# Kernel optimization log

Hardware: AMD Instinct MI355X
Metric: run time of the kernel (lower is better)

The kernel has to match this reference:

```python
import jax, jax.numpy as jnp
import numpy as np

B, C1, C2, H, W = 16, 64, 64, 160, 160
K, KS, HID = 4, 3, 16  # K kernels, 3x3, hidden = max(int(64/16),16)=16
EPS = 1e-5


def setup_inputs() -> dict:
    key = jax.random.key(0)
    ks = jax.random.split(key, 8)
    fan_out = KS * KS * C2
    return {
        "x": jax.random.normal(ks[0], (B, C1, H, W), jnp.float32),
        # K candidate conv kernels and biases
        "Wk": jax.random.normal(ks[1], (K, C2, C1, KS, KS), jnp.float32) * np.sqrt(2.0 / fan_out),
        "bk": jnp.zeros((K, C2), jnp.float32),
        # attention trunk: 1x1 conv C1->HID (no bias), BN, ReLU
        "Wfc": jax.random.normal(ks[2], (HID, C1), jnp.float32) * 0.1,
        "gamma_h": jnp.ones((HID,), jnp.float32),
        "beta_h": jnp.zeros((HID,), jnp.float32),
        # four attention heads
        "Wf": jax.random.normal(ks[3], (C2, HID), jnp.float32) * 0.1,
        "bf": jnp.zeros((C2,), jnp.float32),
        "Ws": jax.random.normal(ks[4], (KS * KS, HID), jnp.float32) * 0.1,
        "bs": jnp.zeros((KS * KS,), jnp.float32),
        "Wc": jax.random.normal(ks[5], (C1, HID), jnp.float32) * 0.1,
        "bc": jnp.zeros((C1,), jnp.float32),
        "Ww": jax.random.normal(ks[6], (K, HID), jnp.float32) * 0.1,
        "bw": jnp.zeros((K,), jnp.float32),
        # outer BatchNorm2d params
        "gamma_o": jnp.ones((C2,), jnp.float32),
        "beta_o": jnp.zeros((C2,), jnp.float32),
    }


def reference(x, Wk, bk, Wfc, gamma_h, beta_h, Wf, bf, Ws, bs, Wc, bc, Ww, bw, gamma_o, beta_o):
    # ---- per-sample attention over K kernels ----
    ctx = x.mean(axis=(2, 3))                      # (B, C1)  global avg pool
    h = ctx @ Wfc.T                                # (B, HID) 1x1 conv == linear
    mu = h.mean(axis=0)
    var = h.var(axis=0)                            # biased, as torch BN training
    h = (h - mu) / jnp.sqrt(var + EPS) * gamma_h + beta_h
    h = jax.nn.relu(h)
    attn_f = jax.nn.sigmoid(h @ Wf.T + bf)         # (B, C2)
    attn_s = jax.nn.sigmoid(h @ Ws.T + bs).reshape(B, KS, KS)
    attn_c = jax.nn.sigmoid(h @ Wc.T + bc)         # (B, C1)
    attn_w = jax.nn.softmax(h @ Ww.T + bw, axis=-1)  # (B, K)

    # attn: (B, K, C2, C1, KS, KS) via broadcasting
    attn = (attn_w[:, :, None, None, None, None]
            * attn_f[:, None, :, None, None, None]
            * attn_c[:, None, None, :, None, None]
            * attn_s[:, None, None, None, :, :])
    weight = jnp.sum(attn * Wk[None], axis=1)      # (B, C2, C1, KS, KS)
    bias = attn_w @ bk                             # (B, C2)

    # ---- batched conv as grouped conv with groups=B ----
    out = jax.lax.conv_general_dilated(
        x.reshape(1, B * C1, H, W),
        weight.reshape(B * C2, C1, KS, KS),
        window_strides=(1, 1), padding=((1, 1), (1, 1)),
        dimension_numbers=('NCHW', 'OIHW', 'NCHW'),
        feature_group_count=B)                     # (1, B*C2, H, W)
    out = out.reshape(B, C2, H, W) + bias[:, :, None, None]

    # ---- outer BatchNorm2d (training stats) + SiLU ----
    mu_o = out.mean(axis=(0, 2, 3))
    var_o = out.var(axis=(0, 2, 3))
    out = (out - mu_o[None, :, None, None]) / jnp.sqrt(var_o + EPS)[None, :, None, None]
    out = out * gamma_o[None, :, None, None] + beta_o[None, :, None, None]
    return out * jax.nn.sigmoid(out)               # SiLU
```

## Files before the change

kernel.cpp:

```cpp
#include <hip/hip_runtime.h>
#include <math.h>

#define BB 16
#define C1 64
#define C2 64
#define HH 160
#define WW 160
#define KK 4
#define HID 16
#define EPS 1e-5f
#define HWSZ (HH*WW)
#define NPB (BB*HWSZ)

#define WS_AF    1024
#define WS_AC    2048
#define WS_AS    3072
#define WS_AW    3216
#define WS_BIAS  3280
#define WS_SC    4304
#define WS_SH    4368
#define WS_STATS 4432
#define NSLOT    32
#define WS_PART  8704
#define WS_WEFF  49664
#define WS_XBF   344576

typedef __attribute__((ext_vector_type(8)))  short bf16x8;
typedef __attribute__((ext_vector_type(16))) float f32x16;

__device__ __forceinline__ unsigned short f2bf(float f) {
    unsigned int u = __float_as_uint(f);
    unsigned int r = (u + 0x7FFFu + ((u >> 16) & 1u)) >> 16;
    return (unsigned short)r;
}

__device__ __forceinline__ void gload16(const void* g, void* l) {
    __builtin_amdgcn_global_load_lds(
        (const __attribute__((address_space(1))) unsigned int*)g,
        (__attribute__((address_space(3))) unsigned int*)l, 16, 0, 0);
}

__global__ __launch_bounds__(256) void xprep_kernel(const float* __restrict__ x,
                                                    float* __restrict__ ws) {
    __shared__ float lds[10240];
    int bcc = blockIdx.y;
    int rg = blockIdx.x;
    int t = threadIdx.x;

    const float* src = x + (size_t)bcc * 16 * HWSZ + (size_t)rg * 4 * WW;
    float4* l4 = (float4*)lds;
    #pragma unroll
    for (int i = 0; i < 10; ++i) {
        int g = i * 256 + t;
        int ch = g / 160, rem = g - ch * 160;
        l4[g] = *(const float4*)(src + (size_t)ch * HWSZ + rem * 4);
    }
    __syncthreads();

    {
        int ch = t >> 4, j = t & 15;
        float s = 0.f;
        #pragma unroll
        for (int m = 0; m < 40; ++m) s += lds[ch * 640 + j + 16 * m];
        #pragma unroll
        for (int o = 8; o > 0; o >>= 1) s += __shfl_down(s, o, 16);
        if (j == 0) ws[WS_PART + ((size_t)bcc * 40 + rg) * 16 + ch] = s;
    }

    uint4* dst = (uint4*)(ws + WS_XBF) + ((size_t)bcc * 160 + rg * 4) * 320;
    #pragma unroll
    for (int i = 0; i < 5; ++i) {
        int u = i * 256 + t;
        int row = u / 320, rem = u - row * 320;
        int col = rem >> 1, p = rem & 1;
        int h = p ^ ((col >> 2) & 1) ^ 1;
        union { uint4 q; unsigned short us[8]; } pk;
        #pragma unroll
        for (int k = 0; k < 8; ++k)
            pk.us[k] = f2bf(lds[(h * 8 + k) * 640 + row * 160 + col]);
        dst[u] = pk.q;
    }
}

__global__ void attn_kernel(float* __restrict__ ws,
    const float* __restrict__ Wfc, const float* __restrict__ gh, const float* __restrict__ bh,
    const float* __restrict__ Wf,  const float* __restrict__ bf,
    const float* __restrict__ Wsm, const float* __restrict__ bs,
    const float* __restrict__ Wc,  const float* __restrict__ bc,
    const float* __restrict__ Ww,  const float* __restrict__ bw,
    const float* __restrict__ bk) {
    __shared__ float ctxs[16][64];
    __shared__ float hs[16][16];
    __shared__ float aw[16][4];
    int t = threadIdx.x;

    #pragma unroll
    for (int q = 0; q < 4; ++q) {
        int idx = t * 4 + q;
        int b = idx >> 6, c1 = idx & 63;
        const float* pp = ws + WS_PART + ((size_t)(b * 4 + (c1 >> 4)) * 40) * 16 + (c1 & 15);
        float s = 0.f;
        #pragma unroll
        for (int rg = 0; rg < 40; ++rg) s += pp[rg * 16];
        ctxs[b][c1] = s * (1.0f / (float)HWSZ);
    }
    __syncthreads();
    {
        int b = t >> 4, j = t & 15;
        const float* wr = Wfc + j * 64;
        float s = 0.f;
        #pragma unroll
        for (int c = 0; c < 64; c++) s += ctxs[b][c] * wr[c];
        hs[b][j] = s;
    }
    __syncthreads();
    if (t < 16) {
        int j = t;
        float mu = 0.f;
        #pragma unroll
        for (int b = 0; b < 16; b++) mu += hs[b][j];
        mu *= (1.f / 16.f);
        float vr = 0.f;
        #pragma unroll
        for (int b = 0; b < 16; b++) { float d = hs[b][j] - mu; vr += d * d; }
        vr *= (1.f / 16.f);
        float sc = gh[j] * rsqrtf(vr + EPS);
        float sh = bh[j] - mu * sc;
        #pragma unroll
        for (int b = 0; b < 16; b++) {
            float v = hs[b][j] * sc + sh;
            hs[b][j] = v > 0.f ? v : 0.f;
        }
    }
    __syncthreads();
    if (t < 16) {
        int b = t;
        float l[4]; float mx = -1e30f;
        #pragma unroll
        for (int k = 0; k < 4; k++) {
            float s = bw[k];
            #pragma unroll
            for (int j = 0; j < 16; j++) s += hs[b][j] * Ww[k * 16 + j];
            l[k] = s; mx = fmaxf(mx, s);
        }
        float den = 0.f;
        #pragma unroll
        for (int k = 0; k < 4; k++) { l[k] = expf(l[k] - mx); den += l[k]; }
        float r = 1.f / den;
        #pragma unroll
        for (int k = 0; k < 4; k++) { float v = l[k] * r; aw[b][k] = v; ws[WS_AW + b * 4 + k] = v; }
    }
    #pragma unroll
    for (int q = 0; q < 4; q++) {
        int idx = t * 4 + q;
        int b = idx >> 6, c2 = idx & 63;
        float sf = bf[c2], sc2 = bc[c2];
        #pragma unroll
        for (int j = 0; j < 16; j++) {
            float hv = hs[b][j];
            sf  += hv * Wf[c2 * 16 + j];
            sc2 += hv * Wc[c2 * 16 + j];
        }
        ws[WS_AF + idx] = 1.f / (1.f + expf(-sf));
        ws[WS_AC + idx] = 1.f / (1.f + expf(-sc2));
    }
    if (t < 144) {
        int b = t / 9, uv = t % 9;
        float s = bs[uv];
        #pragma unroll
        for (int j = 0; j < 16; j++) s += hs[b][j] * Wsm[uv * 16 + j];
        ws[WS_AS + t] = 1.f / (1.f + expf(-s));
    }
    __syncthreads();
    #pragma unroll
    for (int q = 0; q < 4; q++) {
        int idx = t * 4 + q;
        int b = idx >> 6, c2 = idx & 63;
        float s = 0.f;
        #pragma unroll
        for (int k = 0; k < 4; k++) s += aw[b][k] * bk[k * 64 + c2];
        ws[WS_BIAS + idx] = s;
    }
    for (int i = t; i < NSLOT * 128; i += 256) ws[WS_STATS + i] = 0.f;
}

__global__ void wprep_kernel(const float* __restrict__ Wk, float* __restrict__ ws) {
    int b = blockIdx.y;
    int tid = blockIdx.x * 256 + threadIdx.x;
    int h = tid & 1;
    int c2 = (tid >> 1) & 63;
    int g = tid >> 7;
    int uv = g % 9;
    int chunk = g / 9;
    const float* awp = ws + WS_AW + b * 4;
    float aw0 = awp[0], aw1 = awp[1], aw2 = awp[2], aw3 = awp[3];
    float af = ws[WS_AF + b * 64 + c2];
    float as_ = ws[WS_AS + b * 9 + uv];
    union { uint4 q; unsigned short u[8]; } pk;
    #pragma unroll
    for (int j = 0; j < 8; ++j) {
        int c1 = chunk * 16 + h * 8 + j;
        const float* wp = Wk + (size_t)(c2 * 64 + c1) * 9 + uv;
        float s = aw0 * wp[0] + aw1 * wp[64 * 64 * 9] + aw2 * wp[2 * 64 * 64 * 9] + aw3 * wp[3 * 64 * 64 * 9];
        float w = s * af * ws[WS_AC + b * 64 + c1] * as_;
        pk.u[j] = f2bf(w);
    }
    int unit = ((chunk * 9 + uv) * 64 + c2) * 2 + (h ^ ((c2 >> 2) & 1));
    ((uint4*)(ws + WS_WEFF))[(size_t)b * 4608 + unit] = pk.q;
}

__launch_bounds__(256, 2)
__global__ void conv_kernel(const float* __restrict__ wsf, float* __restrict__ out) {
    __shared__ uint4 xs[6 * 162 * 2];
    __shared__ uint4 wsh[2][1152];
    __shared__ float bsh[64];
    __shared__ float sst[128];

    int id = blockIdx.x;
    int b = id & 15;
    int bx = id >> 4;
    int y0 = bx * 4;
    int t = threadIdx.x;
    int wv = t >> 6;
    int lane = t & 63;
    int l31 = lane & 31;
    int l5 = lane >> 5;

    if (t < 64) bsh[t] = wsf[WS_BIAS + b * 64 + t];
    if (t >= 64 && t < 128) sst[t - 64] = 0.f;
    if (t >= 128 && t < 192) sst[t - 64] = 0.f;
    if (t >= 192 && t < 216) {
        int q = t - 192;
        int r = q >> 2, side = (q >> 1) & 1, p = q & 1;
        xs[(r * 162 + side * 161) * 2 + p] = make_uint4(0, 0, 0, 0);
    }
    int rbad = (bx == 0) ? 0 : (bx == 39 ? 5 : -1);
    if (rbad >= 0) {
        for (int i = t; i < 320; i += 256)
            xs[(rbad * 162 + 1) * 2 + i] = make_uint4(0, 0, 0, 0);
    }

    const uint4* weff = (const uint4*)(wsf + WS_WEFF) + (size_t)b * 4608;
    const uint4* xbf  = (const uint4*)(wsf + WS_XBF);

    auto stage_w = [&](int cc, int bq) {
        for (int i = wv; i < 18; i += 4)
            gload16(weff + (size_t)cc * 1152 + i * 64 + lane, (char*)&wsh[bq][0] + i * 1024);
    };
    auto stage_x = [&](int cc) {
        for (int i = wv; i < 30; i += 4) {
            int r = i / 5, seg = i % 5;
            int gy = y0 - 1 + r;
            if (gy >= 0 && gy < HH)
                gload16(xbf + (((size_t)b * 4 + cc) * 160 + gy) * 320 + seg * 64 + lane,
                        (char*)xs + ((r * 162 + 1) * 2 + seg * 64) * 16);
        }
    };

    f32x16 acc[2][5];
    #pragma unroll
    for (int a = 0; a < 2; ++a)
        #pragma unroll
        for (int j = 0; j < 5; ++j)
            #pragma unroll
            for (int r = 0; r < 16; ++r) acc[a][j][r] = 0.f;

    stage_w(0, 0);
    stage_x(0);
    __syncthreads();

    int cur = 0;
    int aswz = (l31 >> 2) & 1;
    for (int cc = 0; cc < 4; ++cc) {
        if (cc < 3) stage_w(cc + 1, cur ^ 1);
        #pragma unroll
        for (int uv = 0; uv < 9; ++uv) {
            bf16x8 a0 = *(bf16x8*)&wsh[cur][(uv * 64 + l31) * 2 + (l5 ^ aswz)];
            bf16x8 a1 = *(bf16x8*)&wsh[cur][(uv * 64 + 32 + l31) * 2 + (l5 ^ aswz)];
            int xrow = wv + uv / 3;
            int v = uv % 3;
            #pragma unroll
            for (int j = 0; j < 5; ++j) {
                int col = j * 32 + l31 + v;
                bf16x8 bb = *(bf16x8*)&xs[(xrow * 162 + col) * 2 + (l5 ^ (((col + 3) >> 2) & 1))];
                acc[0][j] = __builtin_amdgcn_mfma_f32_32x32x16_bf16(a0, bb, acc[0][j], 0, 0, 0);
                acc[1][j] = __builtin_amdgcn_mfma_f32_32x32x16_bf16(a1, bb, acc[1][j], 0, 0, 0);
            }
        }
        __syncthreads();
        if (cc < 3) stage_x(cc + 1);
        __syncthreads();
        cur ^= 1;
    }

    float* outb = out + (size_t)b * C2 * HWSZ + (size_t)(y0 + wv) * WW;
    #pragma unroll
    for (int a = 0; a < 2; ++a) {
        float sr[16], qr[16];
        #pragma unroll
        for (int r = 0; r < 16; ++r) {
            int c2r = a * 32 + (r & 3) + 8 * (r >> 2) + 4 * l5;
            float bias = bsh[c2r];
            float s = 0.f, q = 0.f;
            #pragma unroll
            for (int j = 0; j < 5; ++j) {
                float v = acc[a][j][r] + bias;
                outb[(size_t)c2r * HWSZ + j * 32 + l31] = v;
                s += v;
                q = fmaf(v, v, q);
            }
            sr[r] = s; qr[r] = q;
        }
        #pragma unroll
        for (int k = 0; k < 4; ++k) {
            int m = 1 << k, n = 8 >> k;
            #pragma unroll
            for (int i = 0; i < 8; ++i) {
                if (i < n) {
                    float ks = (l31 & m) ? sr[i + n] : sr[i];
                    float ss = (l31 & m) ? sr[i] : sr[i + n];
                    sr[i] = ks + __shfl_xor(ss, m, 64);
                    float kq = (l31 & m) ? qr[i + n] : qr[i];
                    float sq = (l31 & m) ? qr[i] : qr[i + n];
                    qr[i] = kq + __shfl_xor(sq, m, 64);
                }
            }
        }
        sr[0] += __shfl_xor(sr[0], 16, 64);
        qr[0] += __shfl_xor(qr[0], 16, 64);
        if (l31 < 16) {
            int rf = ((l31 & 1) << 3) | ((l31 & 2) << 1) | ((l31 & 4) >> 1) | ((l31 & 8) >> 3);
            int c2r = a * 32 + (rf & 3) + 8 * (rf >> 2) + 4 * l5;
            atomicAdd(&sst[c2r], sr[0]);
            atomicAdd(&sst[64 + c2r], qr[0]);
        }
    }
    __syncthreads();
    if (t < 128) {
        int slot = id & (NSLOT - 1);
        atomicAdd((float*)wsf + WS_STATS + slot * 128 + t, sst[t]);
    }
}

__global__ void bnstat_kernel(float* __restrict__ ws, const float* __restrict__ go,
                              const float* __restrict__ bo) {
    int c = threadIdx.x;
    float s = 0.f, q = 0.f;
    for (int sl = 0; sl < NSLOT; sl++) {
        s += ws[WS_STATS + sl * 128 + c];
        q += ws[WS_STATS + sl * 128 + 64 + c];
    }
    float mu  = s * (1.0f / (float)NPB);
    float var = q * (1.0f / (float)NPB) - mu * mu;
    float sc  = go[c] * rsqrtf(var + EPS);
    ws[WS_SC + c] = sc;
    ws[WS_SH + c] = bo[c] - mu * sc;
}

__global__ void bnact_kernel(float* __restrict__ out, const float* __restrict__ ws) {
    __shared__ float sc[64], sh[64];
    if (threadIdx.x < 64) {
        sc[threadIdx.x] = ws[WS_SC + threadIdx.x];
        sh[threadIdx.x] = ws[WS_SH + threadIdx.x];
    }
    __syncthreads();
    const int n4 = BB * C2 * HWSZ / 4;
    for (int i = blockIdx.x * blockDim.x + threadIdx.x; i < n4; i += gridDim.x * blockDim.x) {
        float4 v = ((float4*)out)[i];
        int c = ((i * 4) / HWSZ) & 63;
        float s = sc[c], h = sh[c];
        v.x = v.x * s + h; v.y = v.y * s + h; v.z = v.z * s + h; v.w = v.w * s + h;
        v.x = v.x / (1.f + __expf(-v.x));
        v.y = v.y / (1.f + __expf(-v.y));
        v.z = v.z / (1.f + __expf(-v.z));
        v.w = v.w / (1.f + __expf(-v.w));
        ((float4*)out)[i] = v;
    }
}

extern "C" void kernel_launch(void* const* d_in, const int* in_sizes, int n_in,
                              void* d_out, int out_size, void* d_ws, size_t ws_size,
                              hipStream_t stream) {
    const float* x   = (const float*)d_in[0];
    const float* Wk  = (const float*)d_in[1];
    const float* bk  = (const float*)d_in[2];
    const float* Wfc = (const float*)d_in[3];
    const float* gh  = (const float*)d_in[4];
    const float* bh  = (const float*)d_in[5];
    const float* Wf  = (const float*)d_in[6];
    const float* bf  = (const float*)d_in[7];
    const float* Wsm = (const float*)d_in[8];
    const float* bs  = (const float*)d_in[9];
    const float* Wc  = (const float*)d_in[10];
    const float* bc  = (const float*)d_in[11];
    const float* Ww  = (const float*)d_in[12];
    const float* bw  = (const float*)d_in[13];
    const float* go  = (const float*)d_in[14];
    const float* bo  = (const float*)d_in[15];
    float* out = (float*)d_out;
    float* ws  = (float*)d_ws;

    xprep_kernel<<<dim3(40, 64), dim3(256), 0, stream>>>(x, ws);
    attn_kernel<<<dim3(1), dim3(256), 0, stream>>>(ws, Wfc, gh, bh, Wf, bf, Wsm, bs, Wc, bc, Ww, bw, bk);
    wprep_kernel<<<dim3(18, 16), dim3(256), 0, stream>>>(Wk, ws);
    conv_kernel<<<dim3(640), dim3(256), 0, stream>>>(ws, out);
    bnstat_kernel<<<dim3(1), dim3(64), 0, stream>>>(ws, go, bo);
    bnact_kernel<<<dim3(2048), dim3(256), 0, stream>>>(out, ws);
}
```

Baseline: 132.4 us.

## Halve conv tile rows, split output channels across waves, drop double buffering

Measured after the change: 131.4 us. No clear change (-0.7%).

```diff
diff --git a/kernel.cpp b/kernel.cpp
--- a/kernel.cpp
+++ b/kernel.cpp
@@ -209,32 +209,33 @@
     ((uint4*)(ws + WS_WEFF))[(size_t)b * 4608 + unit] = pk.q;
 }
 
-__launch_bounds__(256, 2)
+__launch_bounds__(256, 3)
 __global__ void conv_kernel(const float* __restrict__ wsf, float* __restrict__ out) {
-    __shared__ uint4 xs[6 * 162 * 2];
-    __shared__ uint4 wsh[2][1152];
+    __shared__ uint4 xs[4 * 162 * 2];
+    __shared__ uint4 wsh[1152];
     __shared__ float bsh[64];
     __shared__ float sst[128];
 
     int id = blockIdx.x;
     int b = id & 15;
     int bx = id >> 4;
-    int y0 = bx * 4;
+    int y0 = bx * 2;
     int t = threadIdx.x;
     int wv = t >> 6;
     int lane = t & 63;
     int l31 = lane & 31;
     int l5 = lane >> 5;
+    int c2h = wv & 1;
+    int rw = wv >> 1;
 
     if (t < 64) bsh[t] = wsf[WS_BIAS + b * 64 + t];
-    if (t >= 64 && t < 128) sst[t - 64] = 0.f;
-    if (t >= 128 && t < 192) sst[t - 64] = 0.f;
-    if (t >= 192 && t < 216) {
+    if (t >= 64 && t < 192) sst[t - 64] = 0.f;
+    if (t >= 192 && t < 208) {
         int q = t - 192;
         int r = q >> 2, side = (q >> 1) & 1, p = q & 1;
         xs[(r * 162 + side * 161) * 2 + p] = make_uint4(0, 0, 0, 0);
     }
-    int rbad = (bx == 0) ? 0 : (bx == 39 ? 5 : -1);
+    int rbad = (bx == 0) ? 0 : (bx == 79 ? 3 : -1);
     if (rbad >= 0) {
         for (int i = t; i < 320; i += 256)
             xs[(rbad * 162 + 1) * 2 + i] = make_uint4(0, 0, 0, 0);
@@ -243,97 +244,80 @@
     const uint4* weff = (const uint4*)(wsf + WS_WEFF) + (size_t)b * 4608;
     const uint4* xbf  = (const uint4*)(wsf + WS_XBF);
 
-    auto stage_w = [&](int cc, int bq) {
+    f32x16 acc[5];
+    #pragma unroll
+    for (int j = 0; j < 5; ++j)
+        #pragma unroll
+        for (int r = 0; r < 16; ++r) acc[j][r] = 0.f;
+
+    int c2 = c2h * 32 + l31;
+    int aswz = (l31 >> 2) & 1;
+    for (int cc = 0; cc < 4; ++cc) {
+        __syncthreads();
         for (int i = wv; i < 18; i += 4)
-            gload16(weff + (size_t)cc * 1152 + i * 64 + lane, (char*)&wsh[bq][0] + i * 1024);
-    };
-    auto stage_x = [&](int cc) {
-        for (int i = wv; i < 30; i += 4) {
+            gload16(weff + (size_t)cc * 1152 + i * 64 + lane, (char*)wsh + i * 1024);
+        for (int i = wv; i < 20; i += 4) {
             int r = i / 5, seg = i % 5;
             int gy = y0 - 1 + r;
             if (gy >= 0 && gy < HH)
                 gload16(xbf + (((size_t)b * 4 + cc) * 160 + gy) * 320 + seg * 64 + lane,
                         (char*)xs + ((r * 162 + 1) * 2 + seg * 64) * 16);
         }
-    };
-
-    f32x16 acc[2][5];
-    #pragma unroll
-    for (int a = 0; a < 2; ++a)
-        #pragma unroll
-        for (int j = 0; j < 5; ++j)
-            #pragma unroll
-            for (int r = 0; r < 16; ++r) acc[a][j][r] = 0.f;
-
-    stage_w(0, 0);
-    stage_x(0);
-    __syncthreads();
-
-    int cur = 0;
-    int aswz = (l31 >> 2) & 1;
-    for (int cc = 0; cc < 4; ++cc) {
-        if (cc < 3) stage_w(cc + 1, cur ^ 1);
+        __syncthreads();
+
         #pragma unroll
         for (int uv = 0; uv < 9; ++uv) {
-            bf16x8 a0 = *(bf16x8*)&wsh[cur][(uv * 64 + l31) * 2 + (l5 ^ aswz)];
-            bf16x8 a1 = *(bf16x8*)&wsh[cur][(uv * 64 + 32 + l31) * 2 + (l5 ^ aswz)];
-            int xrow = wv + uv / 3;
+            bf16x8 a = *(bf16x8*)&wsh[(uv * 64 + c2) * 2 + (l5 ^ aswz)];
+            int xr = rw + uv / 3;
             int v = uv % 3;
             #pragma unroll
             for (int j = 0; j < 5; ++j) {
                 int col = j * 32 + l31 + v;
-                bf16x8 bb = *(bf16x8*)&xs[(xrow * 162 + col) * 2 + (l5 ^ (((col + 3) >> 2) & 1))];
-                acc[0][j] = __builtin_amdgcn_mfma_f32_32x32x16_bf16(a0, bb, acc[0][j], 0, 0, 0);
-                acc[1][j] = __builtin_amdgcn_mfma_f32_32x32x16_bf16(a1, bb, acc[1][j], 0, 0, 0);
+                bf16x8 bb = *(bf16x8*)&xs[(xr * 162 + col) * 2 + (l5 ^ (((col + 3) >> 2) & 1))];
+                acc[j] = __builtin_amdgcn_mfma_f32_32x32x16_bf16(a, bb, acc[j], 0, 0, 0);
             }
         }
-        __syncthreads();
-        if (cc < 3) stage_x(cc + 1);
-        __syncthreads();
-        cur ^= 1;
-    }
-
-    float* outb = out + (size_t)b * C2 * HWSZ + (size_t)(y0 + wv) * WW;
-    #pragma unroll
-    for (int a = 0; a < 2; ++a) {
-        float sr[16], qr[16];
-        #pragma unroll
-        for (int r = 0; r < 16; ++r) {
-            int c2r = a * 32 + (r & 3) + 8 * (r >> 2) + 4 * l5;
-            float bias = bsh[c2r];
-            float s = 0.f, q = 0.f;
-            #pragma unroll
-            for (int j = 0; j < 5; ++j) {
-                float v = acc[a][j][r] + bias;
-                outb[(size_t)c2r * HWSZ + j * 32 + l31] = v;
-                s += v;
-                q = fmaf(v, v, q);
+    }
+
+    float* outb = out + (size_t)b * C2 * HWSZ + (size_t)(y0 + rw) * WW;
+    int cb = c2h * 32 + 4 * l5;
+    float sr[16], qr[16];
+    #pragma unroll
+    for (int r = 0; r < 16; ++r) {
+        int c2r = cb + (r & 3) + 8 * (r >> 2);
+        float bias = bsh[c2r];
+        float s = 0.f, q = 0.f;
+        #pragma unroll
+        for (int j = 0; j < 5; ++j) {
+            float v = acc[j][r] + bias;
+            outb[(size_t)c2r * HWSZ + j * 32 + l31] = v;
+            s += v;
+            q = fmaf(v, v, q);
+        }
+        sr[r] = s; qr[r] = q;
+    }
+    #pragma unroll
+    for (int k = 0; k < 4; ++k) {
+        int m = 1 << k, n = 8 >> k;
+        #pragma unroll
+        for (int i = 0; i < 8; ++i) {
+            if (i < n) {
+                float ks = (l31 & m) ? sr[i + n] : sr[i];
+                float ss = (l31 & m) ? sr[i] : sr[i + n];
+                sr[i] = ks + __shfl_xor(ss, m, 64);
+                float kq = (l31 & m) ? qr[i + n] : qr[i];
+                float sq = (l31 & m) ? qr[i] : qr[i + n];
+                qr[i] = kq + __shfl_xor(sq, m, 64);
             }
-            sr[r] = s; qr[r] = q;
-        }
-        #pragma unroll
-        for (int k = 0; k < 4; ++k) {
-            int m = 1 << k, n = 8 >> k;
-            #pragma unroll
-            for (int i = 0; i < 8; ++i) {
-                if (i < n) {
-                    float ks = (l31 & m) ? sr[i + n] : sr[i];
-                    float ss = (l31 & m) ? sr[i] : sr[i + n];
-                    sr[i] = ks + __shfl_xor(ss, m, 64);
-                    float kq = (l31 & m) ? qr[i + n] : qr[i];
-                    float sq = (l31 & m) ? qr[i] : qr[i + n];
-                    qr[i] = kq + __shfl_xor(sq, m, 64);
-                }
-            }
-        }
-        sr[0] += __shfl_xor(sr[0], 16, 64);
-        qr[0] += __shfl_xor(qr[0], 16, 64);
-        if (l31 < 16) {
-            int rf = ((l31 & 1) << 3) | ((l31 & 2) << 1) | ((l31 & 4) >> 1) | ((l31 & 8) >> 3);
-            int c2r = a * 32 + (rf & 3) + 8 * (rf >> 2) + 4 * l5;
-            atomicAdd(&sst[c2r], sr[0]);
-            atomicAdd(&sst[64 + c2r], qr[0]);
-        }
+        }
+    }
+    sr[0] += __shfl_xor(sr[0], 16, 64);
+    qr[0] += __shfl_xor(qr[0], 16, 64);
+    if (l31 < 16) {
+        int rf = ((l31 & 1) << 3) | ((l31 & 2) << 1) | ((l31 & 4) >> 1) | ((l31 & 8) >> 3);
+        int c2r = cb + (rf & 3) + 8 * (rf >> 2);
+        atomicAdd(&sst[c2r], sr[0]);
+        atomicAdd(&sst[64 + c2r], qr[0]);
     }
     __syncthreads();
     if (t < 128) {
@@ -403,7 +387,7 @@
     xprep_kernel<<<dim3(40, 64), dim3(256), 0, stream>>>(x, ws);
     attn_kernel<<<dim3(1), dim3(256), 0, stream>>>(ws, Wfc, gh, bh, Wf, bf, Wsm, bs, Wc, bc, Ww, bw, bk);
     wprep_kernel<<<dim3(18, 16), dim3(256), 0, stream>>>(Wk, ws);
-    conv_kernel<<<dim3(640), dim3(256), 0, stream>>>(ws, out);
+    conv_kernel<<<dim3(1280), dim3(256), 0, stream>>>(ws, out);
     bnstat_kernel<<<dim3(1), dim3(64), 0, stream>>>(ws, go, bo);
     bnact_kernel<<<dim3(2048), dim3(256), 0, stream>>>(out, ws);
 }
```
